# Kernel optimization log

Hardware: AMD Instinct MI355X
Metric: run time of the kernel (lower is better)

## Reference

```python
import jax, jax.numpy as jnp
import numpy as np

B, C, T, F = 256, 1, 8192, 16


def _lrelu(h):
    return jnp.where(h > 0, h, 0.01 * h)


def _adain(h, style):
    # h: (B, T, 8), style: (B, 8, 2)
    scale = style[:, None, :, 0]          # (B, 1, 8)
    bias = style[:, None, :, 1]           # (B, 1, 8)
    mu = jnp.mean(h, axis=-1, keepdims=True)
    sigma = jnp.std(h, axis=-1, ddof=1, keepdims=True) + 1e-6  # torch.std is unbiased
    return scale * (h - mu) / sigma + bias


def setup_inputs() -> dict:
    key = jax.random.key(0)
    ks = jax.random.split(key, 20)
    g = lambda k, shp, s=0.2: (jax.random.normal(k, shp, dtype=jnp.float32) * s)
    inp = {
        "x": jax.random.normal(ks[0], (B, C, T), dtype=jnp.float32),
        "metadata": jax.random.normal(ks[1], (B, F), dtype=jnp.float32),
        # MetadataMLP: F->64->128->64 (total_channels*2 = 32*2)
        "mw1": g(ks[2], (F, 64)), "mb1": g(ks[3], (64,)),
        "mw2": g(ks[4], (64, 128)), "mb2": g(ks[5], (128,)),
        "mw3": g(ks[6], (128, 64)), "mb3": g(ks[7], (64,)),
        # main chain 1->8->8->8->8->1
        "w1": g(ks[8], (1, 8)), "b1": g(ks[9], (8,)),
        "w2": g(ks[10], (8, 8)), "b2": g(ks[11], (8,)),
        "w3": g(ks[12], (8, 8)), "b3": g(ks[13], (8,)),
        "w4": g(ks[14], (8, 8)), "b4": g(ks[15], (8,)),
        "w5": g(ks[16], (8, 1)), "b5": g(ks[17], (1,)),
    }
    return inp


def reference(x, metadata, mw1, mb1, mw2, mb2, mw3, mb3,
              w1, b1, w2, b2, w3, b3, w4, b4, w5, b5):
    # style MLP
    s = jax.nn.relu(metadata @ mw1 + mb1)
    s = jax.nn.relu(s @ mw2 + mb2)
    s = s @ mw3 + mb3                     # (B, 64)
    s1, s2, s3, s4 = jnp.split(s, 4, axis=1)  # each (B, 16)
    s1, s2, s3, s4 = (t.reshape(-1, 8, 2) for t in (s1, s2, s3, s4))

    h = jnp.transpose(x, (0, 2, 1))       # (B, T, 1)
    h = h @ w1 + b1                       # (B, T, 8)
    h = _lrelu(_adain(h, s1))
    h = h @ w2 + b2
    h = _lrelu(_adain(h, s2))
    h = h @ w3 + b3
    h = _lrelu(_adain(h, s3))
    h = h @ w4 + b4
    h = _lrelu(_adain(h, s4))
    h = h @ w5 + b5                       # (B, T, 1)
    out = _lrelu(h)
    return jnp.transpose(out, (0, 2, 1))  # (B, 1, T)
```

## Files before the change

kernel.cpp:

```cpp
#include <hip/hip_runtime.h>

#define BATCH  256
#define TLEN   8192
#define TPB    1024
#define LUTN   1024
#define VLO    -8.0f
#define H      0.015625f
#define INVH   64.0f
#define UOFF   512.0f
#define UMAX   1022.999f
#define SQRT7  2.6457513110645906f
#define C1     2.6457513110645906e-6f


__device__ __forceinline__ float rowmean8(const float* __restrict__ p) {
    return (((p[0] + p[1]) + (p[2] + p[3])) + ((p[4] + p[5]) + (p[6] + p[7]))) * 0.125f;
}
__device__ __forceinline__ float lrelu(float t) { return fmaxf(t, 0.01f * t); }

__global__ __launch_bounds__(TPB, 8) void adain_lut_kernel(
    const float* __restrict__ x, const float* __restrict__ metadata,
    const float* __restrict__ mw1, const float* __restrict__ mb1,
    const float* __restrict__ mw2, const float* __restrict__ mb2,
    const float* __restrict__ mw3, const float* __restrict__ mb3,
    const float* __restrict__ w1, const float* __restrict__ b1,
    const float* __restrict__ w2, const float* __restrict__ b2,
    const float* __restrict__ w3, const float* __restrict__ b3,
    const float* __restrict__ w4, const float* __restrict__ b4,
    const float* __restrict__ w5, const float* __restrict__ b5,
    float* __restrict__ out)
{
    __shared__ float smw1[1024];
    __shared__ float smw2[8192];
    __shared__ float smw3[8192];
    __shared__ float md[16];
    __shared__ float h1[64];
    __shared__ float h2[128];
    __shared__ float s[64];
    __shared__ float la[8], lc[8];
    __shared__ float p[304];
    __shared__ float lut[LUTN];

    const int b   = blockIdx.x;
    const int tid = threadIdx.x;

    const int base4 = b * (TLEN / 4) + tid;
    float4 vx0 = ((const float4*)x)[base4];
    float4 vx1 = ((const float4*)x)[base4 + TPB];

    float4 t2a = ((const float4*)mw2)[tid];
    float4 t2b = ((const float4*)mw2)[tid + TPB];
    float4 t3a = ((const float4*)mw3)[tid];
    float4 t3b = ((const float4*)mw3)[tid + TPB];
    float4 t1  = (tid < 256) ? ((const float4*)mw1)[tid] : make_float4(0.f, 0.f, 0.f, 0.f);

    ((float4*)smw2)[tid]       = t2a;
    ((float4*)smw2)[tid + TPB] = t2b;
    ((float4*)smw3)[tid]       = t3a;
    ((float4*)smw3)[tid + TPB] = t3b;
    if (tid < 256) ((float4*)smw1)[tid] = t1;

    if (tid < 16) {
        md[tid] = metadata[b * 16 + tid];
    } else if (tid >= 128 && tid < 192) {
        int i = tid - 128; p[32 + i]  = w2[i] - rowmean8(w2 + (i & 56));
    } else if (tid >= 192 && tid < 256) {
        int i = tid - 192; p[120 + i] = w3[i] - rowmean8(w3 + (i & 56));
    } else if (tid >= 256 && tid < 320) {
        int i = tid - 256; p[208 + i] = w4[i] - rowmean8(w4 + (i & 56));
    } else if (tid >= 320 && tid < 328) {
        int j = tid - 320; la[j] = w1[j] - rowmean8(w1); lc[j] = b1[j] - rowmean8(b1);
    } else if (tid >= 328 && tid < 336) {
        int j = tid - 328; p[96 + j]  = b2[j] - rowmean8(b2);
    } else if (tid >= 336 && tid < 344) {
        int j = tid - 336; p[184 + j] = b3[j] - rowmean8(b3);
    } else if (tid >= 344 && tid < 352) {
        int j = tid - 344; p[272 + j] = b4[j] - rowmean8(b4);
    } else if (tid >= 352 && tid < 360) {
        int j = tid - 352; p[296 + j] = w5[j];
    } else if (tid == 360) {
        p[27] = b5[0];
    }
    __syncthreads();

    if (tid < 64) {
        float a = mb1[tid];
        #pragma unroll
        for (int k = 0; k < 16; ++k) a = fmaf(md[k], smw1[k * 64 + tid], a);
        h1[tid] = fmaxf(a, 0.f);
    }
    __syncthreads();
    if (tid < 128) {
        float a = mb2[tid];
        #pragma unroll 16
        for (int k = 0; k < 64; ++k) a = fmaf(h1[k], smw2[k * 128 + tid], a);
        h2[tid] = fmaxf(a, 0.f);
    }
    __syncthreads();
    if (tid < 64) {
        float a = mb3[tid];
        #pragma unroll 16
        for (int k = 0; k < 128; ++k) a = fmaf(h2[k], smw3[k * 64 + tid], a);
        s[tid] = a;
    }
    __syncthreads();

    if (tid < 8) {
        const float sc1 = s[2 * tid] * SQRT7;
        p[tid]      = la[tid] * sc1;
        p[8 + tid]  = lc[tid] * sc1;
        p[16 + tid] = s[2 * tid + 1];
        p[104 + tid] = s[16 + 2 * tid] * SQRT7;  p[112 + tid] = s[16 + 2 * tid + 1];
        p[192 + tid] = s[32 + 2 * tid] * SQRT7;  p[200 + tid] = s[32 + 2 * tid + 1];
        p[280 + tid] = s[48 + 2 * tid] * SQRT7;  p[288 + tid] = s[48 + 2 * tid + 1];
    } else if (tid == 8) {
        float A = 0.f, B = 0.f, C = 0.f;
        #pragma unroll
        for (int j = 0; j < 8; ++j) {
            A = fmaf(la[j], la[j], A);
            B = fmaf(la[j], lc[j], B);
            C = fmaf(lc[j], lc[j], C);
        }
        p[24] = A; p[25] = 2.f * B; p[26] = C;
    }
    __syncthreads();

    {
        const float4 q = *(const float4*)(p + 24);
        const float vv = VLO + (float)tid * H;

        float h[8];
        {
            const float4 a0 = *(const float4*)(p);
            const float4 a1 = *(const float4*)(p + 4);
            const float4 c0 = *(const float4*)(p + 8);
            const float4 c1 = *(const float4*)(p + 12);
            const float4 s0 = *(const float4*)(p + 16);
            const float4 s1 = *(const float4*)(p + 20);
            const float laa[8] = {a0.x,a0.y,a0.z,a0.w,a1.x,a1.y,a1.z,a1.w};
            const float lcc[8] = {c0.x,c0.y,c0.z,c0.w,c1.x,c1.y,c1.z,c1.w};
            const float sb1[8] = {s0.x,s0.y,s0.z,s0.w,s1.x,s1.y,s1.z,s1.w};
            const float var = fmaxf(fmaf(vv, fmaf(vv, q.x, q.y), q.z), 0.f);
            const float r   = __builtin_amdgcn_rcpf(__builtin_amdgcn_sqrtf(var) + C1);
            #pragma unroll
            for (int j = 0; j < 8; ++j) {
                const float d = fmaf(vv, laa[j], lcc[j]);
                h[j] = lrelu(fmaf(d, r, sb1[j]));
            }
        }

        #pragma unroll 1
        for (int l = 0; l < 3; ++l) {
            const float* __restrict__ w = p + 32 + l * 88;

            float g[8];
            {
                const float4 c0 = *(const float4*)(w + 64);
                const float4 c1 = *(const float4*)(w + 68);
                const float4 wa = *(const float4*)(w);
                const float4 wb = *(const float4*)(w + 4);
                const float hk = h[0];
                g[0] = fmaf(hk, wa.x, c0.x); g[1] = fmaf(hk, wa.y, c0.y);
                g[2] = fmaf(hk, wa.z, c0.z); g[3] = fmaf(hk, wa.w, c0.w);
                g[4] = fmaf(hk, wb.x, c1.x); g[5] = fmaf(hk, wb.y, c1.y);
                g[6] = fmaf(hk, wb.z, c1.z); g[7] = fmaf(hk, wb.w, c1.w);
            }
            #pragma unroll
            for (int k = 1; k < 8; ++k) {
                const float4 wa = *(const float4*)(w + k * 8);
                const float4 wb = *(const float4*)(w + k * 8 + 4);
                const float hk = h[k];
                g[0] = fmaf(hk, wa.x, g[0]); g[1] = fmaf(hk, wa.y, g[1]);
                g[2] = fmaf(hk, wa.z, g[2]); g[3] = fmaf(hk, wa.w, g[3]);
                g[4] = fmaf(hk, wb.x, g[4]); g[5] = fmaf(hk, wb.y, g[5]);
                g[6] = fmaf(hk, wb.z, g[6]); g[7] = fmaf(hk, wb.w, g[7]);
            }
            {
                const float4 s0 = *(const float4*)(w + 72);
                const float4 s1 = *(const float4*)(w + 76);
                const float4 t0 = *(const float4*)(w + 80);
                const float4 t1 = *(const float4*)(w + 84);
                const float sc[8] = {s0.x,s0.y,s0.z,s0.w,s1.x,s1.y,s1.z,s1.w};
                const float sb[8] = {t0.x,t0.y,t0.z,t0.w,t1.x,t1.y,t1.z,t1.w};
                float var = 0.f;
                #pragma unroll
                for (int j = 0; j < 8; ++j) var = fmaf(g[j], g[j], var);
                const float r = __builtin_amdgcn_rcpf(__builtin_amdgcn_sqrtf(var) + C1);
                #pragma unroll
                for (int j = 0; j < 8; ++j)
                    h[j] = lrelu(fmaf(g[j] * r, sc[j], sb[j]));
            }
        }

        {
            const float4 f0 = *(const float4*)(p + 296);
            const float4 f1 = *(const float4*)(p + 300);
            const float w5v[8] = {f0.x,f0.y,f0.z,f0.w,f1.x,f1.y,f1.z,f1.w};
            float a = q.w;
            #pragma unroll
            for (int k = 0; k < 8; ++k) a = fmaf(h[k], w5v[k], a);
            lut[tid] = lrelu(a);
        }
    }
    __syncthreads();

    #pragma unroll
    for (int r = 0; r < 2; ++r) {
        const float4 v = r ? vx1 : vx0;
        const float vin[4] = {v.x, v.y, v.z, v.w};
        float vo[4];
        #pragma unroll
        for (int c = 0; c < 4; ++c) {
            float u = fmaf(vin[c], INVH, UOFF);
            u = fminf(fmaxf(u, 0.0f), UMAX);
            const int   i = (int)u;
            const float f = u - (float)i;
            const float a = lut[i];
            const float d = lut[i + 1] - a;
            vo[c] = fmaf(f, d, a);
        }
        ((float4*)out)[base4 + r * TPB] = make_float4(vo[0], vo[1], vo[2], vo[3]);
    }
}

extern "C" void kernel_launch(void* const* d_in, const int* in_sizes, int n_in,
                              void* d_out, int out_size, void* d_ws, size_t ws_size,
                              hipStream_t stream)
{
    const float* x        = (const float*)d_in[0];
    const float* metadata = (const float*)d_in[1];
    const float* mw1      = (const float*)d_in[2];
    const float* mb1      = (const float*)d_in[3];
    const float* mw2      = (const float*)d_in[4];
    const float* mb2      = (const float*)d_in[5];
    const float* mw3      = (const float*)d_in[6];
    const float* mb3      = (const float*)d_in[7];
    const float* w1       = (const float*)d_in[8];
    const float* b1       = (const float*)d_in[9];
    const float* w2       = (const float*)d_in[10];
    const float* b2       = (const float*)d_in[11];
    const float* w3       = (const float*)d_in[12];
    const float* b3       = (const float*)d_in[13];
    const float* w4       = (const float*)d_in[14];
    const float* b4       = (const float*)d_in[15];
    const float* w5       = (const float*)d_in[16];
    const float* b5       = (const float*)d_in[17];

    adain_lut_kernel<<<BATCH, TPB, 0, stream>>>(
        x, metadata, mw1, mb1, mw2, mb2, mw3, mb3,
        w1, b1, w2, b2, w3, b3, w4, b4, w5, b5, (float*)d_out);
}
```

Measured before the change: 101.3 us.

## Split LUT construction and LUT application into separate kernels using workspace

Separates the per-batch lookup-table construction into its own kernel that writes tables to the workspace buffer, then launches a lighter apply kernel with four 256-thread blocks per batch row to interpolate the input. This aims to spread the memory-bound apply phase across more blocks and reduce the time each large block holds resources. It adds a second launch and a global-memory round trip for the tables. The original fused kernel is kept as a fallback when no workspace is provided.

```diff
diff --git a/kernel.cpp b/kernel.cpp
--- a/kernel.cpp
+++ b/kernel.cpp
@@ -2,7 +2,9 @@
 
 #define BATCH  256
 #define TLEN   8192
-#define TPB    1024
+#define TPB1   1024
+#define TPB2   256
+#define CHUNKS 4
 #define LUTN   1024
 #define VLO    -8.0f
 #define H      0.015625f
@@ -18,8 +20,9 @@
 }
 __device__ __forceinline__ float lrelu(float t) { return fmaxf(t, 0.01f * t); }
 
-__global__ __launch_bounds__(TPB, 8) void adain_lut_kernel(
-    const float* __restrict__ x, const float* __restrict__ metadata,
+__device__ __forceinline__ float build_lut_point(
+    const int b, const int tid,
+    const float* __restrict__ metadata,
     const float* __restrict__ mw1, const float* __restrict__ mb1,
     const float* __restrict__ mw2, const float* __restrict__ mb2,
     const float* __restrict__ mw3, const float* __restrict__ mb3,
@@ -28,36 +31,20 @@
     const float* __restrict__ w3, const float* __restrict__ b3,
     const float* __restrict__ w4, const float* __restrict__ b4,
     const float* __restrict__ w5, const float* __restrict__ b5,
-    float* __restrict__ out)
-{
-    __shared__ float smw1[1024];
-    __shared__ float smw2[8192];
-    __shared__ float smw3[8192];
-    __shared__ float md[16];
-    __shared__ float h1[64];
-    __shared__ float h2[128];
-    __shared__ float s[64];
-    __shared__ float la[8], lc[8];
-    __shared__ float p[304];
-    __shared__ float lut[LUTN];
-
-    const int b   = blockIdx.x;
-    const int tid = threadIdx.x;
-
-    const int base4 = b * (TLEN / 4) + tid;
-    float4 vx0 = ((const float4*)x)[base4];
-    float4 vx1 = ((const float4*)x)[base4 + TPB];
-
+    float* smw1, float* smw2, float* smw3,
+    float* md, float* h1, float* h2, float* s,
+    float* la, float* lc, float* p)
+{
     float4 t2a = ((const float4*)mw2)[tid];
-    float4 t2b = ((const float4*)mw2)[tid + TPB];
+    float4 t2b = ((const float4*)mw2)[tid + TPB1];
     float4 t3a = ((const float4*)mw3)[tid];
-    float4 t3b = ((const float4*)mw3)[tid + TPB];
+    float4 t3b = ((const float4*)mw3)[tid + TPB1];
     float4 t1  = (tid < 256) ? ((const float4*)mw1)[tid] : make_float4(0.f, 0.f, 0.f, 0.f);
 
-    ((float4*)smw2)[tid]       = t2a;
-    ((float4*)smw2)[tid + TPB] = t2b;
-    ((float4*)smw3)[tid]       = t3a;
-    ((float4*)smw3)[tid + TPB] = t3b;
+    ((float4*)smw2)[tid]        = t2a;
+    ((float4*)smw2)[tid + TPB1] = t2b;
+    ((float4*)smw3)[tid]        = t3a;
+    ((float4*)smw3)[tid + TPB1] = t3b;
     if (tid < 256) ((float4*)smw1)[tid] = t1;
 
     if (tid < 16) {
@@ -125,83 +112,132 @@
     }
     __syncthreads();
 
+    const float4 q = *(const float4*)(p + 24);
+    const float vv = VLO + (float)tid * H;
+
+    float h[8];
     {
-        const float4 q = *(const float4*)(p + 24);
-        const float vv = VLO + (float)tid * H;
-
-        float h[8];
+        const float4 a0 = *(const float4*)(p);
+        const float4 a1 = *(const float4*)(p + 4);
+        const float4 c0 = *(const float4*)(p + 8);
+        const float4 c1 = *(const float4*)(p + 12);
+        const float4 s0 = *(const float4*)(p + 16);
+        const float4 s1 = *(const float4*)(p + 20);
+        const float laa[8] = {a0.x,a0.y,a0.z,a0.w,a1.x,a1.y,a1.z,a1.w};
+        const float lcc[8] = {c0.x,c0.y,c0.z,c0.w,c1.x,c1.y,c1.z,c1.w};
+        const float sb1[8] = {s0.x,s0.y,s0.z,s0.w,s1.x,s1.y,s1.z,s1.w};
+        const float var = fmaxf(fmaf(vv, fmaf(vv, q.x, q.y), q.z), 0.f);
+        const float r   = __builtin_amdgcn_rcpf(__builtin_amdgcn_sqrtf(var) + C1);
+        #pragma unroll
+        for (int j = 0; j < 8; ++j) {
+            const float d = fmaf(vv, laa[j], lcc[j]);
+            h[j] = lrelu(fmaf(d, r, sb1[j]));
+        }
+    }
+
+    #pragma unroll 1
+    for (int l = 0; l < 3; ++l) {
+        const float* __restrict__ w = p + 32 + l * 88;
+
+        float g[8];
         {
-            const float4 a0 = *(const float4*)(p);
-            const float4 a1 = *(const float4*)(p + 4);
-            const float4 c0 = *(const float4*)(p + 8);
-            const float4 c1 = *(const float4*)(p + 12);
-            const float4 s0 = *(const float4*)(p + 16);
-            const float4 s1 = *(const float4*)(p + 20);
-            const float laa[8] = {a0.x,a0.y,a0.z,a0.w,a1.x,a1.y,a1.z,a1.w};
-            const float lcc[8] = {c0.x,c0.y,c0.z,c0.w,c1.x,c1.y,c1.z,c1.w};
-            const float sb1[8] = {s0.x,s0.y,s0.z,s0.w,s1.x,s1.y,s1.z,s1.w};
-            const float var = fmaxf(fmaf(vv, fmaf(vv, q.x, q.y), q.z), 0.f);
-            const float r   = __builtin_amdgcn_rcpf(__builtin_amdgcn_sqrtf(var) + C1);
+            const float4 c0 = *(const float4*)(w + 64);
+            const float4 c1 = *(const float4*)(w + 68);
+            const float4 wa = *(const float4*)(w);
+            const float4 wb = *(const float4*)(w + 4);
+            const float hk = h[0];
+            g[0] = fmaf(hk, wa.x, c0.x); g[1] = fmaf(hk, wa.y, c0.y);
+            g[2] = fmaf(hk, wa.z, c0.z); g[3] = fmaf(hk, wa.w, c0.w);
+            g[4] = fmaf(hk, wb.x, c1.x); g[5] = fmaf(hk, wb.y, c1.y);
+            g[6] = fmaf(hk, wb.z, c1.z); g[7] = fmaf(hk, wb.w, c1.w);
+        }
+        #pragma unroll
+        for (int k = 1; k < 8; ++k) {
+            const float4 wa = *(const float4*)(w + k * 8);
+            const float4 wb = *(const float4*)(w + k * 8 + 4);
+            const float hk = h[k];
+            g[0] = fmaf(hk, wa.x, g[0]); g[1] = fmaf(hk, wa.y, g[1]);
+            g[2] = fmaf(hk, wa.z, g[2]); g[3] = fmaf(hk, wa.w, g[3]);
+            g[4] = fmaf(hk, wb.x, g[4]); g[5] = fmaf(hk, wb.y, g[5]);
+            g[6] = fmaf(hk, wb.z, g[6]); g[7] = fmaf(hk, wb.w, g[7]);
+        }
+        {
+            const float4 s0 = *(const float4*)(w + 72);
+            const float4 s1 = *(const float4*)(w + 76);
+            const float4 t0 = *(const float4*)(w + 80);
+            const float4 t1 = *(const float4*)(w + 84);
+            const float sc[8] = {s0.x,s0.y,s0.z,s0.w,s1.x,s1.y,s1.z,s1.w};
+            const float sb[8] = {t0.x,t0.y,t0.z,t0.w,t1.x,t1.y,t1.z,t1.w};
+            float var = 0.f;
             #pragma unroll
-            for (int j = 0; j < 8; ++j) {
-                const float d = fmaf(vv, laa[j], lcc[j]);
-                h[j] = lrelu(fmaf(d, r, sb1[j]));
-            }
-        }
-
-        #pragma unroll 1
-        for (int l = 0; l < 3; ++l) {
-            const float* __restrict__ w = p + 32 + l * 88;
-
-            float g[8];
-            {
-                const float4 c0 = *(const float4*)(w + 64);
-                const float4 c1 = *(const float4*)(w + 68);
-                const float4 wa = *(const float4*)(w);
-                const float4 wb = *(const float4*)(w + 4);
-                const float hk = h[0];
-                g[0] = fmaf(hk, wa.x, c0.x); g[1] = fmaf(hk, wa.y, c0.y);
-                g[2] = fmaf(hk, wa.z, c0.z); g[3] = fmaf(hk, wa.w, c0.w);
-                g[4] = fmaf(hk, wb.x, c1.x); g[5] = fmaf(hk, wb.y, c1.y);
-                g[6] = fmaf(hk, wb.z, c1.z); g[7] = fmaf(hk, wb.w, c1.w);
-            }
+            for (int j = 0; j < 8; ++j) var = fmaf(g[j], g[j], var);
+            const float r = __builtin_amdgcn_rcpf(__builtin_amdgcn_sqrtf(var) + C1);
             #pragma unroll
-            for (int k = 1; k < 8; ++k) {
-                const float4 wa = *(const float4*)(w + k * 8);
-                const float4 wb = *(const float4*)(w + k * 8 + 4);
-                const float hk = h[k];
-                g[0] = fmaf(hk, wa.x, g[0]); g[1] = fmaf(hk, wa.y, g[1]);
-                g[2] = fmaf(hk, wa.z, g[2]); g[3] = fmaf(hk, wa.w, g[3]);
-                g[4] = fmaf(hk, wb.x, g[4]); g[5] = fmaf(hk, wb.y, g[5]);
-                g[6] = fmaf(hk, wb.z, g[6]); g[7] = fmaf(hk, wb.w, g[7]);
-            }
-            {
-                const float4 s0 = *(const float4*)(w + 72);
-                const float4 s1 = *(const float4*)(w + 76);
-                const float4 t0 = *(const float4*)(w + 80);
-                const float4 t1 = *(const float4*)(w + 84);
-                const float sc[8] = {s0.x,s0.y,s0.z,s0.w,s1.x,s1.y,s1.z,s1.w};
-                const float sb[8] = {t0.x,t0.y,t0.z,t0.w,t1.x,t1.y,t1.z,t1.w};
-                float var = 0.f;
-                #pragma unroll
-                for (int j = 0; j < 8; ++j) var = fmaf(g[j], g[j], var);
-                const float r = __builtin_amdgcn_rcpf(__builtin_amdgcn_sqrtf(var) + C1);
-                #pragma unroll
-                for (int j = 0; j < 8; ++j)
-                    h[j] = lrelu(fmaf(g[j] * r, sc[j], sb[j]));
-            }
-        }
-
-        {
-            const float4 f0 = *(const float4*)(p + 296);
-            const float4 f1 = *(const float4*)(p + 300);
-            const float w5v[8] = {f0.x,f0.y,f0.z,f0.w,f1.x,f1.y,f1.z,f1.w};
-            float a = q.w;
-            #pragma unroll
-            for (int k = 0; k < 8; ++k) a = fmaf(h[k], w5v[k], a);
-            lut[tid] = lrelu(a);
-        }
-    }
+            for (int j = 0; j < 8; ++j)
+                h[j] = lrelu(fmaf(g[j] * r, sc[j], sb[j]));
+        }
+    }
+
+    {
+        const float4 f0 = *(const float4*)(p + 296);
+        const float4 f1 = *(const float4*)(p + 300);
+        const float w5v[8] = {f0.x,f0.y,f0.z,f0.w,f1.x,f1.y,f1.z,f1.w};
+        float a = q.w;
+        #pragma unroll
+        for (int k = 0; k < 8; ++k) a = fmaf(h[k], w5v[k], a);
+        return lrelu(a);
+    }
+}
+
+__global__ __launch_bounds__(TPB1, 8) void lut_build_kernel(
+    const float* __restrict__ metadata,
+    const float* __restrict__ mw1, const float* __restrict__ mb1,
+    const float* __restrict__ mw2, const float* __restrict__ mb2,
+    const float* __restrict__ mw3, const float* __restrict__ mb3,
+    const float* __restrict__ w1, const float* __restrict__ b1,
+    const float* __restrict__ w2, const float* __restrict__ b2,
+    const float* __restrict__ w3, const float* __restrict__ b3,
+    const float* __restrict__ w4, const float* __restrict__ b4,
+    const float* __restrict__ w5, const float* __restrict__ b5,
+    float* __restrict__ lut_out)
+{
+    __shared__ float smw1[1024];
+    __shared__ float smw2[8192];
+    __shared__ float smw3[8192];
+    __shared__ float md[16];
+    __shared__ float h1[64];
+    __shared__ float h2[128];
+    __shared__ float s[64];
+    __shared__ float la[8], lc[8];
+    __shared__ float p[304];
+
+    const int b   = blockIdx.x;
+    const int tid = threadIdx.x;
+
+    const float lv = build_lut_point(b, tid, metadata, mw1, mb1, mw2, mb2,
+                                     mw3, mb3, w1, b1, w2, b2, w3, b3,
+                                     w4, b4, w5, b5,
+                                     smw1, smw2, smw3, md, h1, h2, s, la, lc, p);
+    lut_out[b * LUTN + tid] = lv;
+}
+
+__global__ __launch_bounds__(TPB2, 8) void apply_kernel(
+    const float* __restrict__ x, const float* __restrict__ lut_in,
+    float* __restrict__ out)
+{
+    __shared__ float lut[LUTN];
+
+    const int b   = blockIdx.x >> 2;
+    const int q   = blockIdx.x & 3;
+    const int tid = threadIdx.x;
+
+    const float4 lv = ((const float4*)(lut_in + b * LUTN))[tid];
+
+    const int base4 = b * (TLEN / 4) + q * (TLEN / 4 / CHUNKS) + tid;
+    const float4 vx0 = ((const float4*)x)[base4];
+    const float4 vx1 = ((const float4*)x)[base4 + TPB2];
+
+    ((float4*)lut)[tid] = lv;
     __syncthreads();
 
     #pragma unroll
@@ -219,7 +255,63 @@
             const float d = lut[i + 1] - a;
             vo[c] = fmaf(f, d, a);
         }
-        ((float4*)out)[base4 + r * TPB] = make_float4(vo[0], vo[1], vo[2], vo[3]);
+        ((float4*)out)[base4 + r * TPB2] = make_float4(vo[0], vo[1], vo[2], vo[3]);
+    }
+}
+
+__global__ __launch_bounds__(TPB1, 8) void adain_lut_fused_kernel(
+    const float* __restrict__ x, const float* __restrict__ metadata,
+    const float* __restrict__ mw1, const float* __restrict__ mb1,
+    const float* __restrict__ mw2, const float* __restrict__ mb2,
+    const float* __restrict__ mw3, const float* __restrict__ mb3,
+    const float* __restrict__ w1, const float* __restrict__ b1,
+    const float* __restrict__ w2, const float* __restrict__ b2,
+    const float* __restrict__ w3, const float* __restrict__ b3,
+    const float* __restrict__ w4, const float* __restrict__ b4,
+    const float* __restrict__ w5, const float* __restrict__ b5,
+    float* __restrict__ out)
+{
+    __shared__ float smw1[1024];
+    __shared__ float smw2[8192];
+    __shared__ float smw3[8192];
+    __shared__ float md[16];
+    __shared__ float h1[64];
+    __shared__ float h2[128];
+    __shared__ float s[64];
+    __shared__ float la[8], lc[8];
+    __shared__ float p[304];
+    __shared__ float lut[LUTN];
+
+    const int b   = blockIdx.x;
+    const int tid = threadIdx.x;
+
+    const int base4 = b * (TLEN / 4) + tid;
+    float4 vx0 = ((const float4*)x)[base4];
+    float4 vx1 = ((const float4*)x)[base4 + TPB1];
+
+    const float lv = build_lut_point(b, tid, metadata, mw1, mb1, mw2, mb2,
+                                     mw3, mb3, w1, b1, w2, b2, w3, b3,
+                                     w4, b4, w5, b5,
+                                     smw1, smw2, smw3, md, h1, h2, s, la, lc, p);
+    lut[tid] = lv;
+    __syncthreads();
+
+    #pragma unroll
+    for (int r = 0; r < 2; ++r) {
+        const float4 v = r ? vx1 : vx0;
+        const float vin[4] = {v.x, v.y, v.z, v.w};
+        float vo[4];
+        #pragma unroll
+        for (int c = 0; c < 4; ++c) {
+            float u = fmaf(vin[c], INVH, UOFF);
+            u = fminf(fmaxf(u, 0.0f), UMAX);
+            const int   i = (int)u;
+            const float f = u - (float)i;
+            const float a = lut[i];
+            const float d = lut[i + 1] - a;
+            vo[c] = fmaf(f, d, a);
+        }
+        ((float4*)out)[base4 + r * TPB1] = make_float4(vo[0], vo[1], vo[2], vo[3]);
     }
 }
 
@@ -246,7 +338,17 @@
     const float* w5       = (const float*)d_in[16];
     const float* b5       = (const float*)d_in[17];
 
-    adain_lut_kernel<<<BATCH, TPB, 0, stream>>>(
-        x, metadata, mw1, mb1, mw2, mb2, mw3, mb3,
-        w1, b1, w2, b2, w3, b3, w4, b4, w5, b5, (float*)d_out);
-}
+    const size_t lut_bytes = (size_t)BATCH * LUTN * sizeof(float);
+
+    if (d_ws != nullptr && ws_size >= lut_bytes) {
+        float* lut_ws = (float*)d_ws;
+        lut_build_kernel<<<BATCH, TPB1, 0, stream>>>(
+            metadata, mw1, mb1, mw2, mb2, mw3, mb3,
+            w1, b1, w2, b2, w3, b3, w4, b4, w5, b5, lut_ws);
+        apply_kernel<<<BATCH * CHUNKS, TPB2, 0, stream>>>(x, lut_ws, (float*)d_out);
+    } else {
+        adain_lut_fused_kernel<<<BATCH, TPB1, 0, stream>>>(
+            x, metadata, mw1, mb1, mw2, mb2, mw3, mb3,
+            w1, b1, w2, b2, w3, b3, w4, b4, w5, b5, (float*)d_out);
+    }
+}
```

After: 104.3 us. 3.0% more time.
